# Performance work log

Measured on AMD Instinct MI355X. Metric: run time of the kernel, lower is better.

## Reference

```python
import jax, jax.numpy as jnp
import numpy as np

NP_CONST = 48.0  # Np in the original code


def dft_matrices(freq=48, time=512):
    # A[t, f] = exp(-2j*pi*t*f/time)/sqrt(time), split into re/im, shape [time, freq]
    t = np.arange(time)[:, None]
    f = np.arange(freq)[None, :]
    ang = -2.0 * np.pi * t * f / time
    scale = 1.0 / np.sqrt(time)
    return (np.cos(ang) * scale).astype(np.float32), (np.sin(ang) * scale).astype(np.float32)


def _mm(xr, xi, wr, wi):
    # complex matmul: (xr + i xi) @ (wr + i wi)
    return xr @ wr - xi @ wi, xr @ wi + xi @ wr


def _act(R, sigma, theta):
    # scaled soft-threshold (standard LAMP shrinkage); returns f and df/dR
    lam = theta[0] * sigma
    mag = jnp.abs(R)
    shr = jnp.maximum(mag - lam, 0.0)
    f = theta[1] * jnp.sign(R) * shr
    df = theta[1] * (mag > lam).astype(R.dtype)
    return f, df


def setup_inputs() -> dict:
    key = jax.random.key(0)
    L, B = 8, 8192
    dre, dim = dft_matrices(48, 512)
    u = jax.random.normal(key, (B, 48, 2), dtype=jnp.float32)
    # per-layer params initialized to the DFT matrices (as in LAMP_layer.__init__)
    A_re = jnp.broadcast_to(jnp.asarray(dre), (L, 512, 48)).copy()
    A_im = jnp.broadcast_to(jnp.asarray(dim), (L, 512, 48)).copy()
    theta = jnp.broadcast_to(jnp.array([1.0, 1.0, -1.0], dtype=jnp.float32), (L, 3)).copy()
    return {"u": u, "A_re": A_re, "A_im": A_im, "theta": theta,
            "DFT_re": jnp.asarray(dre), "DFT_im": jnp.asarray(dim)}


def _lamp_forward(u, A_re, A_im, theta, DFT_re, DFT_im):
    u_re, u_im = u[:, :, 0], u[:, :, 1]          # [B, 48]
    B = u_re.shape[0]
    z_re, z_im = u_re, u_im
    H_re = jnp.zeros((B, 512), dtype=u.dtype)
    H_im = jnp.zeros((B, 512), dtype=u.dtype)

    def layer(carry, params):
        z_re, z_im, H_re, H_im = carry
        Are, Aim, th = params                      # [512,48], [512,48], [3]
        # Z = z @ A.T : [B,48] x [48,512]
        Z_re, Z_im = _mm(z_re, z_im, Are.T, Aim.T)
        R_re = H_re + Z_re
        R_im = H_im + Z_im
        sigma = jnp.sqrt(jnp.sum(z_re * z_re) + jnp.sum(z_im * z_im)) / jnp.sqrt(NP_CONST)
        Hn_re, d_re = _act(R_re, sigma, th)
        Hn_im, d_im = _act(R_im, sigma, th)
        b_re = d_re.sum() / NP_CONST
        b_im = d_im.sum() / NP_CONST
        # h_hat = H_hat @ A : [B,512] x [512,48]
        h_re, h_im = _mm(Hn_re, Hn_im, Are, Aim)
        zn_re = u_re - h_re + b_re * z_re
        zn_im = u_im - h_im + b_im * z_im
        return (zn_re, zn_im, Hn_re, Hn_im), None

    (z_re, z_im, H_re, H_im), _ = jax.lax.scan(layer, (z_re, z_im, H_re, H_im),
                                               (A_re, A_im, theta))
    h_re, h_im = _mm(H_re, H_im, DFT_re, DFT_im)   # [B, 48]
    return jnp.stack((h_re, h_im), axis=2)          # [B, 48, 2]


def reference(u, A_re, A_im, theta, DFT_re, DFT_im):
    return _lamp_forward(u, A_re, A_im, theta, DFT_re, DFT_im)
```

## Files before the change

kernel.cpp:

```cpp
#include <hip/hip_runtime.h>
#include <hip/hip_bf16.h>
#include <math.h>

#define B_   8192
#define F_   48
#define T_   512
#define L_   8
#define NBLK 512
#define THR  256
#define NW   4
#define RPB  16
#define HST  520
#define ZS   52

typedef unsigned short ushort_t;
typedef unsigned int   uint_t;
typedef __attribute__((ext_vector_type(8))) short short8;
typedef __attribute__((ext_vector_type(4))) float f32x4;

#define MFMA(a,b,c) __builtin_amdgcn_mfma_f32_16x16x32_bf16(a,b,c,0,0,0)

__device__ inline ushort_t f2bf(float x) {
    __hip_bfloat16 h = __float2bfloat16(x);
    return *reinterpret_cast<ushort_t*>(&h);
}
__device__ inline float bf2f(ushort_t x) {
    __hip_bfloat16 h;
    *reinterpret_cast<ushort_t*>(&h) = x;
    return __bfloat162float(h);
}
__device__ inline short8 negbf(short8 v) {
    short8 r;
    #pragma unroll
    for (int i = 0; i < 8; ++i) r[i] = v[i] ^ (short)0x8000;
    return r;
}
__device__ inline short8 pack8(float4 a, float4 b) {
    short8 r;
    r[0]=(short)f2bf(a.x); r[1]=(short)f2bf(a.y); r[2]=(short)f2bf(a.z); r[3]=(short)f2bf(a.w);
    r[4]=(short)f2bf(b.x); r[5]=(short)f2bf(b.y); r[6]=(short)f2bf(b.z); r[7]=(short)f2bf(b.w);
    return r;
}

template<int NQ>
__device__ inline void reduce_vals(float* v, float* redL, int wave, int lane) {
    #pragma unroll
    for (int s = 32; s > 0; s >>= 1)
        #pragma unroll
        for (int q = 0; q < NQ; ++q) v[q] += __shfl_xor(v[q], s, 64);
    __syncthreads();
    if (lane == 0)
        #pragma unroll
        for (int q = 0; q < NQ; ++q) redL[q * NW + wave] = v[q];
    __syncthreads();
}

__device__ inline void bar_add(uint_t* cnt, int blk) {
    __hip_atomic_fetch_add(&cnt[(blk & 15) * 32], 1u, __ATOMIC_RELEASE, __HIP_MEMORY_SCOPE_AGENT);
}
__device__ inline void bar_wait(uint_t* cnt, uint_t tgt) {
    if (threadIdx.x == 0) {
        for (;;) {
            uint_t s = 0;
            #pragma unroll
            for (int i = 0; i < 16; ++i)
                s += __hip_atomic_load(&cnt[i * 32], __ATOMIC_RELAXED, __HIP_MEMORY_SCOPE_AGENT);
            if (s >= tgt) break;
            __builtin_amdgcn_s_sleep(2);
        }
        (void)__hip_atomic_load(&cnt[0], __ATOMIC_ACQUIRE, __HIP_MEMORY_SCOPE_AGENT);
    }
    __syncthreads();
}
__device__ inline float aload(const float* p) {
    return __hip_atomic_load(p, __ATOMIC_RELAXED, __HIP_MEMORY_SCOPE_AGENT);
}
__device__ inline void astore(float* p, float v) {
    __hip_atomic_store(p, v, __ATOMIC_RELAXED, __HIP_MEMORY_SCOPE_AGENT);
}

__device__ inline uint_t act2(uint_t v, float lam, float th1, float& cnt_) {
    float lo = __uint_as_float(v << 16);
    float hi = __uint_as_float(v & 0xffff0000u);
    float ml = fabsf(lo), mh = fabsf(hi);
    float fl = th1 * copysignf(fmaxf(ml - lam, 0.f), lo);
    float fh = th1 * copysignf(fmaxf(mh - lam, 0.f), hi);
    cnt_ += ((ml > lam) ? 1.f : 0.f) + ((mh > lam) ? 1.f : 0.f);
    return ((uint_t)f2bf(fl)) | (((uint_t)f2bf(fh)) << 16);
}

__global__ __launch_bounds__(256) void k_pre(
    const float* __restrict__ Ar, const float* __restrict__ Ai,
    const float* __restrict__ Dr, const float* __restrict__ Di,
    ushort_t* __restrict__ Afr, ushort_t* __restrict__ Afi,
    ushort_t* __restrict__ Atr, ushort_t* __restrict__ Ati,
    ushort_t* __restrict__ Dfr, ushort_t* __restrict__ Dfi,
    uint_t* __restrict__ cnt)
{
    const int gt = blockIdx.x * 256 + threadIdx.x;
    const int gs = gridDim.x * 256;
    if (gt < 512) cnt[gt] = 0u;
    for (int idx = gt; idx < L_ * 32768; idx += gs) {
        int j = idx & 7, rest = idx >> 3;
        int mm = rest & 15; rest >>= 4;
        int qq = rest & 3;  rest >>= 2;
        int k2 = rest & 1;  rest >>= 1;
        int tile = rest & 31;
        int l = rest >> 5;
        int t = tile * 16 + mm, k = k2 * 32 + qq * 8 + j;
        float vr = 0.f, vi = 0.f;
        if (k < 48) { int g = l * 24576 + t * 48 + k; vr = Ar[g]; vi = Ai[g]; }
        Afr[idx] = f2bf(vr); Afi[idx] = f2bf(vi);
    }
    for (int idx = gt; idx < L_ * 24576; idx += gs) {
        int j = idx & 7, rest = idx >> 3;
        int mm = rest & 15; rest >>= 4;
        int qq = rest & 3;  rest >>= 2;
        int ks = rest & 15; rest >>= 4;
        int ft = rest % 3;
        int l = rest / 3;
        int f = ft * 16 + mm, k = ks * 32 + qq * 8 + j;
        int g = l * 24576 + k * 48 + f;
        Atr[idx] = f2bf(Ar[g]); Ati[idx] = f2bf(Ai[g]);
    }
    for (int idx = gt; idx < 24576; idx += gs) {
        int j = idx & 7, rest = idx >> 3;
        int mm = rest & 15; rest >>= 4;
        int qq = rest & 3;  rest >>= 2;
        int ks = rest & 15;
        int ft = rest >> 4;
        int f = ft * 16 + mm, k = ks * 32 + qq * 8 + j;
        Dfr[idx] = f2bf(Dr[k * 48 + f]); Dfi[idx] = f2bf(Di[k * 48 + f]);
    }
}

__device__ inline void fwd_gemm(const ushort_t* Aflr, const ushort_t* Afli,
    const float* zreL, const float* zimL, ushort_t* HreL, ushort_t* HimL,
    int wave, int lane, int quad, int m, bool addH)
{
    const float* zpr = zreL + m * ZS;
    const float* zpi = zimL + m * ZS;
    short8 zr0 = pack8(*(const float4*)(zpr + quad * 8), *(const float4*)(zpr + quad * 8 + 4));
    short8 zi0 = pack8(*(const float4*)(zpi + quad * 8), *(const float4*)(zpi + quad * 8 + 4));
    short8 zr1 = {0,0,0,0,0,0,0,0}, zi1 = {0,0,0,0,0,0,0,0};
    if (quad < 2) {
        zr1 = pack8(*(const float4*)(zpr + 32 + quad * 8), *(const float4*)(zpr + 36 + quad * 8));
        zi1 = pack8(*(const float4*)(zpi + 32 + quad * 8), *(const float4*)(zpi + 36 + quad * 8));
    }
    short8 zin0 = negbf(zi0), zin1 = negbf(zi1);
    #pragma unroll
    for (int ct = 0; ct < 8; ++ct) {
        const int tile = wave * 8 + ct;
        const ushort_t* rp = Aflr + (size_t)(tile * 2) * 512 + lane * 8;
        const ushort_t* ip = Afli + (size_t)(tile * 2) * 512 + lane * 8;
        short8 ar0 = *(const short8*)rp;
        short8 ar1 = *(const short8*)(rp + 512);
        short8 ai0 = *(const short8*)ip;
        short8 ai1 = *(const short8*)(ip + 512);
        f32x4 accR = {0.f,0.f,0.f,0.f}, accI = {0.f,0.f,0.f,0.f};
        accR = MFMA(zr0, ar0, accR);
        accR = MFMA(zr1, ar1, accR);
        accR = MFMA(zin0, ai0, accR);
        accR = MFMA(zin1, ai1, accR);
        accI = MFMA(zr0, ai0, accI);
        accI = MFMA(zr1, ai1, accI);
        accI = MFMA(zi0, ar0, accI);
        accI = MFMA(zi1, ar1, accI);
        const int t = tile * 16 + m;
        #pragma unroll
        for (int reg = 0; reg < 4; ++reg) {
            const int lr = quad * 4 + reg;
            float Rr = accR[reg], Ri = accI[reg];
            if (addH) { Rr += bf2f(HreL[lr * HST + t]); Ri += bf2f(HimL[lr * HST + t]); }
            HreL[lr * HST + t] = f2bf(Rr);
            HimL[lr * HST + t] = f2bf(Ri);
        }
    }
    __syncthreads();
}

__global__ __launch_bounds__(THR, 2) void k_lamp(
    const float* __restrict__ u,
    const ushort_t* __restrict__ Afr, const ushort_t* __restrict__ Afi,
    const ushort_t* __restrict__ Atr, const ushort_t* __restrict__ Ati,
    const ushort_t* __restrict__ Dfr, const ushort_t* __restrict__ Dfi,
    const float* __restrict__ th,
    float* part, uint_t* cnt,
    float* __restrict__ out)
{
    extern __shared__ char dyn[];
    float*    pR   = (float*)dyn;
    float*    pI   = pR + 2 * 3 * 16 * 17;
    float*    zreL = pI + 2 * 3 * 16 * 17;
    float*    zimL = zreL + RPB * ZS;
    float*    redL = zimL + RPB * ZS;
    ushort_t* HreL = (ushort_t*)(redL + 32);
    ushort_t* HimL = HreL + RPB * HST;

    const int tid = threadIdx.x, blk = blockIdx.x;
    const int row0 = blk * RPB;
    const int wave = tid >> 6, lane = tid & 63;
    const int quad = lane >> 4, m = lane & 15;
    const int kq = wave;
    const float2* u2 = (const float2*)u;
    uint_t tgt = NBLK;

    {
        float acc = 0.f;
        #pragma unroll
        for (int k3 = 0; k3 < 3; ++k3) {
            int j = tid + k3 * THR;
            int r = j / 48, c = j - r * 48;
            float2 v = u2[(row0 + r) * 48 + c];
            zreL[r * ZS + c] = v.x; zimL[r * ZS + c] = v.y;
            acc += v.x * v.x + v.y * v.y;
        }
        float v[1] = {acc};
        reduce_vals<1>(v, redL, wave, lane);
        if (tid == 0) {
            float t0 = redL[0] + redL[1] + redL[2] + redL[3];
            astore(&part[blk * 8], t0);
        }
        __syncthreads();
        if (tid == 0) bar_add(cnt, blk);
    }

    fwd_gemm(Afr, Afi, zreL, zimL, HreL, HimL, wave, lane, quad, m, false);

    bar_wait(cnt, tgt);
    float lam, th1;
    {
        float v[1];
        v[0] = aload(&part[tid * 8]) + aload(&part[(tid + 256) * 8]);
        reduce_vals<1>(v, redL, wave, lane);
        float sig2 = redL[0] + redL[1] + redL[2] + redL[3];
        lam = th[0] * sqrtf(sig2 * (1.0f / 48.0f));
        th1 = th[1];
    }

    float dR[3], dI[3];
    for (int l = 0; l < L_; ++l) {
        float cr = 0.f, ci = 0.f;
        {
            uint4* Hr4 = (uint4*)HreL;
            uint4* Hi4 = (uint4*)HimL;
            #pragma unroll
            for (int k4 = 0; k4 < 4; ++k4) {
                int j = tid + k4 * THR;
                int r = j >> 6, c4 = j & 63;
                uint4* pr = Hr4 + r * 65 + c4;
                uint4* pi = Hi4 + r * 65 + c4;
                uint4 xr = *pr, xi = *pi;
                xr.x = act2(xr.x, lam, th1, cr); xr.y = act2(xr.y, lam, th1, cr);
                xr.z = act2(xr.z, lam, th1, cr); xr.w = act2(xr.w, lam, th1, cr);
                xi.x = act2(xi.x, lam, th1, ci); xi.y = act2(xi.y, lam, th1, ci);
                xi.z = act2(xi.z, lam, th1, ci); xi.w = act2(xi.w, lam, th1, ci);
                *pr = xr; *pi = xi;
            }
        }
        __syncthreads();
        if (l == L_ - 1) break;

        {
            const ushort_t* Atlr = Atr + (size_t)l * 24576;
            const ushort_t* Atli = Ati + (size_t)l * 24576;
            f32x4 aR[3], aI[3];
            #pragma unroll
            for (int q = 0; q < 3; ++q) { aR[q] = (f32x4){0,0,0,0}; aI[q] = (f32x4){0,0,0,0}; }
            #pragma unroll
            for (int ks = 0; ks < 4; ++ks) {
                const int ksa = kq * 4 + ks;
                const int k0 = ksa * 32 + quad * 8;
                short8 hr = *(const short8*)&HreL[m * HST + k0];
                short8 hi = *(const short8*)&HimL[m * HST + k0];
                short8 hin = negbf(hi);
                #pragma unroll
                for (int ft = 0; ft < 3; ++ft) {
                    short8 br = *(const short8*)(Atlr + (size_t)((ft * 16 + ksa) * 64 + lane) * 8);
                    short8 bi = *(const short8*)(Atli + (size_t)((ft * 16 + ksa) * 64 + lane) * 8);
                    aR[ft] = MFMA(hr, br, aR[ft]);
                    aR[ft] = MFMA(hin, bi, aR[ft]);
                    aI[ft] = MFMA(hr, bi, aI[ft]);
                    aI[ft] = MFMA(hi, br, aI[ft]);
                }
            }
            const int s = kq & 1;
            if (kq < 2) {
                #pragma unroll
                for (int ft = 0; ft < 3; ++ft)
                    #pragma unroll
                    for (int reg = 0; reg < 4; ++reg) {
                        pR[((s * 3 + ft) * 16 + quad * 4 + reg) * 17 + m] = aR[ft][reg];
                        pI[((s * 3 + ft) * 16 + quad * 4 + reg) * 17 + m] = aI[ft][reg];
                    }
            }
            __syncthreads();
            if (kq >= 2) {
                #pragma unroll
                for (int ft = 0; ft < 3; ++ft)
                    #pragma unroll
                    for (int reg = 0; reg < 4; ++reg) {
                        pR[((s * 3 + ft) * 16 + quad * 4 + reg) * 17 + m] += aR[ft][reg];
                        pI[((s * 3 + ft) * 16 + quad * 4 + reg) * 17 + m] += aI[ft][reg];
                    }
            }
            __syncthreads();
        }

        float S1 = 0.f, S2r = 0.f, S2i = 0.f, S3r = 0.f, S3i = 0.f;
        #pragma unroll
        for (int k3 = 0; k3 < 3; ++k3) {
            int j = tid + k3 * THR;
            int r = j / 48, f = j - r * 48;
            int ft = f >> 4, c = f & 15;
            float hR = pR[(ft * 16 + r) * 17 + c] + pR[((3 + ft) * 16 + r) * 17 + c];
            float hI = pI[(ft * 16 + r) * 17 + c] + pI[((3 + ft) * 16 + r) * 17 + c];
            float2 uv = u2[(row0 + r) * 48 + f];
            float zr = zreL[r * ZS + f], zi = zimL[r * ZS + f];
            float dr = uv.x - hR, di = uv.y - hI;
            dR[k3] = dr; dI[k3] = di;
            S1  += dr * dr + di * di;
            S2r += dr * zr; S2i += di * zi;
            S3r += zr * zr; S3i += zi * zi;
        }
        {
            float v[7] = {cr, ci, S1, S2r, S2i, S3r, S3i};
            reduce_vals<7>(v, redL, wave, lane);
            if (tid < 7) {
                float t0 = redL[tid * NW] + redL[tid * NW + 1] + redL[tid * NW + 2] + redL[tid * NW + 3];
                astore(&part[blk * 8 + tid], t0);
            }
            __syncthreads();
            if (tid == 0) bar_add(cnt, blk);
            tgt += NBLK;
        }
        bar_wait(cnt, tgt);
        float bre, bim;
        {
            float v[7];
            #pragma unroll
            for (int q = 0; q < 7; ++q)
                v[q] = aload(&part[tid * 8 + q]) + aload(&part[(tid + 256) * 8 + q]);
            reduce_vals<7>(v, redL, wave, lane);
            float tot[7];
            #pragma unroll
            for (int q = 0; q < 7; ++q)
                tot[q] = redL[q * NW] + redL[q * NW + 1] + redL[q * NW + 2] + redL[q * NW + 3];
            bre = th1 * tot[0] * (1.0f / 48.0f);
            bim = th1 * tot[1] * (1.0f / 48.0f);
            float sig2 = tot[2] + 2.f * bre * tot[3] + 2.f * bim * tot[4]
                       + bre * bre * tot[5] + bim * bim * tot[6];
            lam = th[(l + 1) * 3] * sqrtf(sig2 * (1.0f / 48.0f));
            th1 = th[(l + 1) * 3 + 1];
        }
        #pragma unroll
        for (int k3 = 0; k3 < 3; ++k3) {
            int j = tid + k3 * THR;
            int r = j / 48, f = j - r * 48;
            float zr = zreL[r * ZS + f], zi = zimL[r * ZS + f];
            zreL[r * ZS + f] = dR[k3] + bre * zr;
            zimL[r * ZS + f] = dI[k3] + bim * zi;
        }
        __syncthreads();
        fwd_gemm(Afr + (size_t)(l + 1) * 32768, Afi + (size_t)(l + 1) * 32768,
                 zreL, zimL, HreL, HimL, wave, lane, quad, m, true);
    }

    {
        f32x4 fR[3], fI[3];
        #pragma unroll
        for (int q = 0; q < 3; ++q) { fR[q] = (f32x4){0,0,0,0}; fI[q] = (f32x4){0,0,0,0}; }
        #pragma unroll
        for (int ks = 0; ks < 4; ++ks) {
            const int ksa = kq * 4 + ks;
            const int k0 = ksa * 32 + quad * 8;
            short8 hr = *(const short8*)&HreL[m * HST + k0];
            short8 hi = *(const short8*)&HimL[m * HST + k0];
            short8 hin = negbf(hi);
            #pragma unroll
            for (int ft = 0; ft < 3; ++ft) {
                short8 br = *(const short8*)(Dfr + (size_t)((ft * 16 + ksa) * 64 + lane) * 8);
                short8 bi = *(const short8*)(Dfi + (size_t)((ft * 16 + ksa) * 64 + lane) * 8);
                fR[ft] = MFMA(hr, br, fR[ft]);
                fR[ft] = MFMA(hin, bi, fR[ft]);
                fI[ft] = MFMA(hr, bi, fI[ft]);
                fI[ft] = MFMA(hi, br, fI[ft]);
            }
        }
        const int s = kq & 1;
        if (kq < 2) {
            #pragma unroll
            for (int ft = 0; ft < 3; ++ft)
                #pragma unroll
                for (int reg = 0; reg < 4; ++reg) {
                    pR[((s * 3 + ft) * 16 + quad * 4 + reg) * 17 + m] = fR[ft][reg];
                    pI[((s * 3 + ft) * 16 + quad * 4 + reg) * 17 + m] = fI[ft][reg];
                }
        }
        __syncthreads();
        if (kq >= 2) {
            #pragma unroll
            for (int ft = 0; ft < 3; ++ft)
                #pragma unroll
                for (int reg = 0; reg < 4; ++reg) {
                    pR[((s * 3 + ft) * 16 + quad * 4 + reg) * 17 + m] += fR[ft][reg];
                    pI[((s * 3 + ft) * 16 + quad * 4 + reg) * 17 + m] += fI[ft][reg];
                }
        }
        __syncthreads();
        float2* out2 = (float2*)out;
        #pragma unroll
        for (int k3 = 0; k3 < 3; ++k3) {
            int j = tid + k3 * THR;
            int r = j / 48, f = j - r * 48;
            int ft = f >> 4, c = f & 15;
            float hR = pR[(ft * 16 + r) * 17 + c] + pR[((3 + ft) * 16 + r) * 17 + c];
            float hI = pI[(ft * 16 + r) * 17 + c] + pI[((3 + ft) * 16 + r) * 17 + c];
            out2[(row0 + r) * 48 + f] = make_float2(hR, hI);
        }
    }
}

extern "C" void kernel_launch(void* const* d_in, const int* in_sizes, int n_in,
                              void* d_out, int out_size, void* d_ws, size_t ws_size,
                              hipStream_t stream) {
    (void)in_sizes; (void)n_in; (void)out_size; (void)ws_size;
    const float* u  = (const float*)d_in[0];
    const float* Ar = (const float*)d_in[1];
    const float* Ai = (const float*)d_in[2];
    const float* th = (const float*)d_in[3];
    const float* Dr = (const float*)d_in[4];
    const float* Di = (const float*)d_in[5];
    float* out = (float*)d_out;

    char* p = (char*)d_ws;
    auto alloc = [&](size_t bytes) -> char* {
        char* r = p;
        p += (bytes + 255) & ~(size_t)255;
        return r;
    };
    float*    part = (float*)alloc((size_t)NBLK * 8 * 4);
    uint_t*   cnt  = (uint_t*)alloc(512 * 4);
    ushort_t* Afr = (ushort_t*)alloc((size_t)L_ * 32768 * 2);
    ushort_t* Afi = (ushort_t*)alloc((size_t)L_ * 32768 * 2);
    ushort_t* Atr = (ushort_t*)alloc((size_t)L_ * 24576 * 2);
    ushort_t* Ati = (ushort_t*)alloc((size_t)L_ * 24576 * 2);
    ushort_t* Dfr = (ushort_t*)alloc((size_t)24576 * 2);
    ushort_t* Dfi = (ushort_t*)alloc((size_t)24576 * 2);

    k_pre<<<256, 256, 0, stream>>>(Ar, Ai, Dr, Di, Afr, Afi, Atr, Ati, Dfr, Dfi, cnt);

    const uint_t lds_bytes = 53120;
    hipFuncSetAttribute((const void*)k_lamp,
                        hipFuncAttributeMaxDynamicSharedMemorySize, (int)lds_bytes);
    void* args[] = { (void*)&u, (void*)&Afr, (void*)&Afi, (void*)&Atr, (void*)&Ati,
                     (void*)&Dfr, (void*)&Dfi, (void*)&th,
                     (void*)&part, (void*)&cnt, (void*)&out };
    hipLaunchCooperativeKernel((void*)k_lamp, dim3(NBLK), dim3(THR), args,
                               lds_bytes, stream);
}
```

Before: 292.1 us.

## Split forward GEMM by linearity to overlap with grid barrier wait

The new z is d + b·z, so the forward product is split into a d·A part computed before the grid-wide barrier wait and a (b·z)·A part computed after the scalars b are known. This hides barrier latency behind MFMA work. The soft-threshold activation is also fused into the epilogue of the second GEMM, which removes a separate pass over H in LDS. In exchange the forward GEMM runs twice per layer, there are extra bf16 roundings of H and of the partial operands, and LDS use grows, which could affect occupancy at two blocks per CU.

```diff
diff --git a/kernel.cpp b/kernel.cpp
--- a/kernel.cpp
+++ b/kernel.cpp
@@ -134,9 +134,9 @@
     }
 }
 
-__device__ inline void fwd_gemm(const ushort_t* Aflr, const ushort_t* Afli,
+__device__ inline void fwd_gemm0(const ushort_t* Aflr, const ushort_t* Afli,
     const float* zreL, const float* zimL, ushort_t* HreL, ushort_t* HimL,
-    int wave, int lane, int quad, int m, bool addH)
+    int wave, int lane, int quad, int m)
 {
     const float* zpr = zreL + m * ZS;
     const float* zpi = zimL + m * ZS;
@@ -170,10 +170,8 @@
         #pragma unroll
         for (int reg = 0; reg < 4; ++reg) {
             const int lr = quad * 4 + reg;
-            float Rr = accR[reg], Ri = accI[reg];
-            if (addH) { Rr += bf2f(HreL[lr * HST + t]); Ri += bf2f(HimL[lr * HST + t]); }
-            HreL[lr * HST + t] = f2bf(Rr);
-            HimL[lr * HST + t] = f2bf(Ri);
+            HreL[lr * HST + t] = f2bf(accR[reg]);
+            HimL[lr * HST + t] = f2bf(accI[reg]);
         }
     }
     __syncthreads();
@@ -194,7 +192,11 @@
     float*    zreL = pI + 2 * 3 * 16 * 17;
     float*    zimL = zreL + RPB * ZS;
     float*    redL = zimL + RPB * ZS;
-    ushort_t* HreL = (ushort_t*)(redL + 32);
+    ushort_t* dbr  = (ushort_t*)(redL + 32);
+    ushort_t* dbi  = dbr + 16 * 64;
+    ushort_t* zbr  = dbi + 16 * 64;
+    ushort_t* zbi  = zbr + 16 * 64;
+    ushort_t* HreL = zbi + 16 * 64;
     ushort_t* HimL = HreL + RPB * HST;
 
     const int tid = threadIdx.x, blk = blockIdx.x;
@@ -206,26 +208,28 @@
     uint_t tgt = NBLK;
 
     {
+        int r = tid >> 4, c = 48 + (tid & 15);
+        dbr[r * 64 + c] = 0; dbi[r * 64 + c] = 0;
+        zbr[r * 64 + c] = 0; zbi[r * 64 + c] = 0;
         float acc = 0.f;
         #pragma unroll
         for (int k3 = 0; k3 < 3; ++k3) {
             int j = tid + k3 * THR;
-            int r = j / 48, c = j - r * 48;
-            float2 v = u2[(row0 + r) * 48 + c];
-            zreL[r * ZS + c] = v.x; zimL[r * ZS + c] = v.y;
+            int rr = j / 48, cc = j - rr * 48;
+            float2 v = u2[(row0 + rr) * 48 + cc];
+            zreL[rr * ZS + cc] = v.x; zimL[rr * ZS + cc] = v.y;
             acc += v.x * v.x + v.y * v.y;
         }
         float v[1] = {acc};
         reduce_vals<1>(v, redL, wave, lane);
         if (tid == 0) {
-            float t0 = redL[0] + redL[1] + redL[2] + redL[3];
-            astore(&part[blk * 8], t0);
+            astore(&part[blk * 8], redL[0] + redL[1] + redL[2] + redL[3]);
         }
         __syncthreads();
         if (tid == 0) bar_add(cnt, blk);
     }
 
-    fwd_gemm(Afr, Afi, zreL, zimL, HreL, HimL, wave, lane, quad, m, false);
+    fwd_gemm0(Afr, Afi, zreL, zimL, HreL, HimL, wave, lane, quad, m);
 
     bar_wait(cnt, tgt);
     float lam, th1;
@@ -238,29 +242,28 @@
         th1 = th[1];
     }
 
+    float cr = 0.f, ci = 0.f;
+    {
+        uint4* Hr4 = (uint4*)HreL;
+        uint4* Hi4 = (uint4*)HimL;
+        #pragma unroll
+        for (int k4 = 0; k4 < 4; ++k4) {
+            int j = tid + k4 * THR;
+            int r = j >> 6, c4 = j & 63;
+            uint4* pr = Hr4 + r * 65 + c4;
+            uint4* pi = Hi4 + r * 65 + c4;
+            uint4 xr = *pr, xi = *pi;
+            xr.x = act2(xr.x, lam, th1, cr); xr.y = act2(xr.y, lam, th1, cr);
+            xr.z = act2(xr.z, lam, th1, cr); xr.w = act2(xr.w, lam, th1, cr);
+            xi.x = act2(xi.x, lam, th1, ci); xi.y = act2(xi.y, lam, th1, ci);
+            xi.z = act2(xi.z, lam, th1, ci); xi.w = act2(xi.w, lam, th1, ci);
+            *pr = xr; *pi = xi;
+        }
+        __syncthreads();
+    }
+
     float dR[3], dI[3];
-    for (int l = 0; l < L_; ++l) {
-        float cr = 0.f, ci = 0.f;
-        {
-            uint4* Hr4 = (uint4*)HreL;
-            uint4* Hi4 = (uint4*)HimL;
-            #pragma unroll
-            for (int k4 = 0; k4 < 4; ++k4) {
-                int j = tid + k4 * THR;
-                int r = j >> 6, c4 = j & 63;
-                uint4* pr = Hr4 + r * 65 + c4;
-                uint4* pi = Hi4 + r * 65 + c4;
-                uint4 xr = *pr, xi = *pi;
-                xr.x = act2(xr.x, lam, th1, cr); xr.y = act2(xr.y, lam, th1, cr);
-                xr.z = act2(xr.z, lam, th1, cr); xr.w = act2(xr.w, lam, th1, cr);
-                xi.x = act2(xi.x, lam, th1, ci); xi.y = act2(xi.y, lam, th1, ci);
-                xi.z = act2(xi.z, lam, th1, ci); xi.w = act2(xi.w, lam, th1, ci);
-                *pr = xr; *pi = xi;
-            }
-        }
-        __syncthreads();
-        if (l == L_ - 1) break;
-
+    for (int l = 0; l < L_ - 1; ++l) {
         {
             const ushort_t* Atlr = Atr + (size_t)l * 24576;
             const ushort_t* Atli = Ati + (size_t)l * 24576;
@@ -319,6 +322,8 @@
             float zr = zreL[r * ZS + f], zi = zimL[r * ZS + f];
             float dr = uv.x - hR, di = uv.y - hI;
             dR[k3] = dr; dI[k3] = di;
+            dbr[r * 64 + f] = f2bf(dr);
+            dbi[r * 64 + f] = f2bf(di);
             S1  += dr * dr + di * di;
             S2r += dr * zr; S2i += di * zi;
             S3r += zr * zr; S3i += zi * zi;
@@ -334,6 +339,43 @@
             if (tid == 0) bar_add(cnt, blk);
             tgt += NBLK;
         }
+
+        {
+            const ushort_t* Aflr = Afr + (size_t)(l + 1) * 32768;
+            const ushort_t* Afli = Afi + (size_t)(l + 1) * 32768;
+            short8 dr0 = *(const short8*)&dbr[m * 64 + quad * 8];
+            short8 dr1 = *(const short8*)&dbr[m * 64 + 32 + quad * 8];
+            short8 di0 = *(const short8*)&dbi[m * 64 + quad * 8];
+            short8 di1 = *(const short8*)&dbi[m * 64 + 32 + quad * 8];
+            short8 din0 = negbf(di0), din1 = negbf(di1);
+            #pragma unroll
+            for (int ct = 0; ct < 8; ++ct) {
+                const int tile = wave * 8 + ct;
+                const ushort_t* rp = Aflr + (size_t)(tile * 2) * 512 + lane * 8;
+                const ushort_t* ip = Afli + (size_t)(tile * 2) * 512 + lane * 8;
+                short8 ar0 = *(const short8*)rp;
+                short8 ar1 = *(const short8*)(rp + 512);
+                short8 ai0 = *(const short8*)ip;
+                short8 ai1 = *(const short8*)(ip + 512);
+                f32x4 accR = {0.f,0.f,0.f,0.f}, accI = {0.f,0.f,0.f,0.f};
+                accR = MFMA(dr0, ar0, accR);
+                accR = MFMA(dr1, ar1, accR);
+                accR = MFMA(din0, ai0, accR);
+                accR = MFMA(din1, ai1, accR);
+                accI = MFMA(dr0, ai0, accI);
+                accI = MFMA(dr1, ai1, accI);
+                accI = MFMA(di0, ar0, accI);
+                accI = MFMA(di1, ar1, accI);
+                const int t = tile * 16 + m;
+                #pragma unroll
+                for (int reg = 0; reg < 4; ++reg) {
+                    const int lr = quad * 4 + reg;
+                    HreL[lr * HST + t] = f2bf(bf2f(HreL[lr * HST + t]) + accR[reg]);
+                    HimL[lr * HST + t] = f2bf(bf2f(HimL[lr * HST + t]) + accI[reg]);
+                }
+            }
+        }
+
         bar_wait(cnt, tgt);
         float bre, bim;
         {
@@ -353,17 +395,64 @@
             lam = th[(l + 1) * 3] * sqrtf(sig2 * (1.0f / 48.0f));
             th1 = th[(l + 1) * 3 + 1];
         }
+
         #pragma unroll
         for (int k3 = 0; k3 < 3; ++k3) {
             int j = tid + k3 * THR;
             int r = j / 48, f = j - r * 48;
             float zr = zreL[r * ZS + f], zi = zimL[r * ZS + f];
-            zreL[r * ZS + f] = dR[k3] + bre * zr;
-            zimL[r * ZS + f] = dI[k3] + bim * zi;
+            float zhr = bre * zr, zhi = bim * zi;
+            zbr[r * 64 + f] = f2bf(zhr);
+            zbi[r * 64 + f] = f2bf(zhi);
+            zreL[r * ZS + f] = dR[k3] + zhr;
+            zimL[r * ZS + f] = dI[k3] + zhi;
         }
         __syncthreads();
-        fwd_gemm(Afr + (size_t)(l + 1) * 32768, Afi + (size_t)(l + 1) * 32768,
-                 zreL, zimL, HreL, HimL, wave, lane, quad, m, true);
+
+        cr = 0.f; ci = 0.f;
+        {
+            const ushort_t* Aflr = Afr + (size_t)(l + 1) * 32768;
+            const ushort_t* Afli = Afi + (size_t)(l + 1) * 32768;
+            short8 zr0 = *(const short8*)&zbr[m * 64 + quad * 8];
+            short8 zr1 = *(const short8*)&zbr[m * 64 + 32 + quad * 8];
+            short8 zi0 = *(const short8*)&zbi[m * 64 + quad * 8];
+            short8 zi1 = *(const short8*)&zbi[m * 64 + 32 + quad * 8];
+            short8 zin0 = negbf(zi0), zin1 = negbf(zi1);
+            #pragma unroll
+            for (int ct = 0; ct < 8; ++ct) {
+                const int tile = wave * 8 + ct;
+                const ushort_t* rp = Aflr + (size_t)(tile * 2) * 512 + lane * 8;
+                const ushort_t* ip = Afli + (size_t)(tile * 2) * 512 + lane * 8;
+                short8 ar0 = *(const short8*)rp;
+                short8 ar1 = *(const short8*)(rp + 512);
+                short8 ai0 = *(const short8*)ip;
+                short8 ai1 = *(const short8*)(ip + 512);
+                f32x4 accR = {0.f,0.f,0.f,0.f}, accI = {0.f,0.f,0.f,0.f};
+                accR = MFMA(zr0, ar0, accR);
+                accR = MFMA(zr1, ar1, accR);
+                accR = MFMA(zin0, ai0, accR);
+                accR = MFMA(zin1, ai1, accR);
+                accI = MFMA(zr0, ai0, accI);
+                accI = MFMA(zr1, ai1, accI);
+                accI = MFMA(zi0, ar0, accI);
+                accI = MFMA(zi1, ar1, accI);
+                const int t = tile * 16 + m;
+                #pragma unroll
+                for (int reg = 0; reg < 4; ++reg) {
+                    const int lr = quad * 4 + reg;
+                    float Rr = bf2f(HreL[lr * HST + t]) + accR[reg];
+                    float Ri = bf2f(HimL[lr * HST + t]) + accI[reg];
+                    float mr = fabsf(Rr), mi = fabsf(Ri);
+                    float fr = th1 * copysignf(fmaxf(mr - lam, 0.f), Rr);
+                    float fi = th1 * copysignf(fmaxf(mi - lam, 0.f), Ri);
+                    cr += (mr > lam) ? 1.f : 0.f;
+                    ci += (mi > lam) ? 1.f : 0.f;
+                    HreL[lr * HST + t] = f2bf(fr);
+                    HimL[lr * HST + t] = f2bf(fi);
+                }
+            }
+            __syncthreads();
+        }
     }
 
     {
@@ -450,7 +539,7 @@
 
     k_pre<<<256, 256, 0, stream>>>(Ar, Ai, Dr, Di, Afr, Afi, Atr, Ati, Dfr, Dfi, cnt);
 
-    const uint_t lds_bytes = 53120;
+    const uint_t lds_bytes = 61312;
     hipFuncSetAttribute((const void*)k_lamp,
                         hipFuncAttributeMaxDynamicSharedMemorySize, (int)lds_bytes);
     void* args[] = { (void*)&u, (void*)&Afr, (void*)&Afi, (void*)&Atr, (void*)&Ati,
```

Result: faster. 279.1 us (-4.5%).

## Overlap forward GEMM with grid barrier via linearity split, fuse activation, use smaller blocks

Applied to the files above, without the earlier changes.

Uses linearity to split the forward GEMM of the next layer's z into two parts. The residual part (u - h) goes through the A-GEMM before the grid barrier, and the b*z part is added after the barrier, together with a fused soft-threshold activation. The backward GEMM is reorganized so each of three waves owns one output tile, which removes the two-stage LDS reduction. When occupancy allows, the kernel is templated to run 8 rows per block across 1024 blocks, with a wider sharded barrier counter. This trades twice the forward MFMA work per layer and extra bf16 rounding (from summing separately rounded parts) for hiding the barrier latency and gaining more parallelism.

```diff
diff --git a/kernel.cpp b/kernel.cpp
--- a/kernel.cpp
+++ b/kernel.cpp
@@ -6,12 +6,10 @@
 #define F_   48
 #define T_   512
 #define L_   8
-#define NBLK 512
 #define THR  256
 #define NW   4
-#define RPB  16
 #define HST  520
-#define ZS   52
+#define DST  72
 
 typedef unsigned short ushort_t;
 typedef unsigned int   uint_t;
@@ -35,12 +33,6 @@
     for (int i = 0; i < 8; ++i) r[i] = v[i] ^ (short)0x8000;
     return r;
 }
-__device__ inline short8 pack8(float4 a, float4 b) {
-    short8 r;
-    r[0]=(short)f2bf(a.x); r[1]=(short)f2bf(a.y); r[2]=(short)f2bf(a.z); r[3]=(short)f2bf(a.w);
-    r[4]=(short)f2bf(b.x); r[5]=(short)f2bf(b.y); r[6]=(short)f2bf(b.z); r[7]=(short)f2bf(b.w);
-    return r;
-}
 
 template<int NQ>
 __device__ inline void reduce_vals(float* v, float* redL, int wave, int lane) {
@@ -55,15 +47,18 @@
     __syncthreads();
 }
 
+template<int SH>
 __device__ inline void bar_add(uint_t* cnt, int blk) {
-    __hip_atomic_fetch_add(&cnt[(blk & 15) * 32], 1u, __ATOMIC_RELEASE, __HIP_MEMORY_SCOPE_AGENT);
-}
+    __hip_atomic_fetch_add(&cnt[(blk & (SH - 1)) * 32], 1u, __ATOMIC_RELEASE,
+                           __HIP_MEMORY_SCOPE_AGENT);
+}
+template<int SH>
 __device__ inline void bar_wait(uint_t* cnt, uint_t tgt) {
     if (threadIdx.x == 0) {
         for (;;) {
             uint_t s = 0;
             #pragma unroll
-            for (int i = 0; i < 16; ++i)
+            for (int i = 0; i < SH; ++i)
                 s += __hip_atomic_load(&cnt[i * 32], __ATOMIC_RELAXED, __HIP_MEMORY_SCOPE_AGENT);
             if (s >= tgt) break;
             __builtin_amdgcn_s_sleep(2);
@@ -99,7 +94,7 @@
 {
     const int gt = blockIdx.x * 256 + threadIdx.x;
     const int gs = gridDim.x * 256;
-    if (gt < 512) cnt[gt] = 0u;
+    if (gt < 1024) cnt[gt] = 0u;
     for (int idx = gt; idx < L_ * 32768; idx += gs) {
         int j = idx & 7, rest = idx >> 3;
         int mm = rest & 15; rest >>= 4;
@@ -134,19 +129,58 @@
     }
 }
 
-__device__ inline void fwd_gemm(const ushort_t* Aflr, const ushort_t* Afli,
-    const float* zreL, const float* zimL, ushort_t* HreL, ushort_t* HimL,
-    int wave, int lane, int quad, int m, bool addH)
+template<int RPB, bool ADDH>
+__device__ inline void gemmA(const ushort_t* Aflr, const ushort_t* Afli,
+    const ushort_t* dbr, const ushort_t* dbi, ushort_t* HreL, ushort_t* HimL,
+    int wave, int lane, int quad, int m)
 {
-    const float* zpr = zreL + m * ZS;
-    const float* zpi = zimL + m * ZS;
-    short8 zr0 = pack8(*(const float4*)(zpr + quad * 8), *(const float4*)(zpr + quad * 8 + 4));
-    short8 zi0 = pack8(*(const float4*)(zpi + quad * 8), *(const float4*)(zpi + quad * 8 + 4));
-    short8 zr1 = {0,0,0,0,0,0,0,0}, zi1 = {0,0,0,0,0,0,0,0};
-    if (quad < 2) {
-        zr1 = pack8(*(const float4*)(zpr + 32 + quad * 8), *(const float4*)(zpr + 36 + quad * 8));
-        zi1 = pack8(*(const float4*)(zpi + 32 + quad * 8), *(const float4*)(zpi + 36 + quad * 8));
-    }
+    short8 dr0 = *(const short8*)&dbr[m * DST + quad * 8];
+    short8 dr1 = *(const short8*)&dbr[m * DST + 32 + quad * 8];
+    short8 di0 = *(const short8*)&dbi[m * DST + quad * 8];
+    short8 di1 = *(const short8*)&dbi[m * DST + 32 + quad * 8];
+    short8 din0 = negbf(di0), din1 = negbf(di1);
+    #pragma unroll
+    for (int ct = 0; ct < 8; ++ct) {
+        const int tile = wave * 8 + ct;
+        const ushort_t* rp = Aflr + (size_t)(tile * 2) * 512 + lane * 8;
+        const ushort_t* ip = Afli + (size_t)(tile * 2) * 512 + lane * 8;
+        short8 ar0 = *(const short8*)rp;
+        short8 ar1 = *(const short8*)(rp + 512);
+        short8 ai0 = *(const short8*)ip;
+        short8 ai1 = *(const short8*)(ip + 512);
+        f32x4 accR = {0.f,0.f,0.f,0.f}, accI = {0.f,0.f,0.f,0.f};
+        accR = MFMA(dr0, ar0, accR);
+        accR = MFMA(dr1, ar1, accR);
+        accR = MFMA(din0, ai0, accR);
+        accR = MFMA(din1, ai1, accR);
+        accI = MFMA(dr0, ai0, accI);
+        accI = MFMA(dr1, ai1, accI);
+        accI = MFMA(di0, ar0, accI);
+        accI = MFMA(di1, ar1, accI);
+        const int t = tile * 16 + m;
+        #pragma unroll
+        for (int reg = 0; reg < 4; ++reg) {
+            const int lr = quad * 4 + reg;
+            if (RPB == 16 || lr < RPB) {
+                float Rr = accR[reg], Ri = accI[reg];
+                if (ADDH) { Rr += bf2f(HreL[lr * HST + t]); Ri += bf2f(HimL[lr * HST + t]); }
+                HreL[lr * HST + t] = f2bf(Rr);
+                HimL[lr * HST + t] = f2bf(Ri);
+            }
+        }
+    }
+}
+
+template<int RPB>
+__device__ inline void gemmB(const ushort_t* Aflr, const ushort_t* Afli,
+    const ushort_t* dbr, const ushort_t* dbi, ushort_t* HreL, ushort_t* HimL,
+    float lam, float th1, float& cr, float& ci,
+    int wave, int lane, int quad, int m)
+{
+    short8 zr0 = *(const short8*)&dbr[m * DST + quad * 8];
+    short8 zr1 = *(const short8*)&dbr[m * DST + 32 + quad * 8];
+    short8 zi0 = *(const short8*)&dbi[m * DST + quad * 8];
+    short8 zi1 = *(const short8*)&dbi[m * DST + 32 + quad * 8];
     short8 zin0 = negbf(zi0), zin1 = negbf(zi1);
     #pragma unroll
     for (int ct = 0; ct < 8; ++ct) {
@@ -170,15 +204,54 @@
         #pragma unroll
         for (int reg = 0; reg < 4; ++reg) {
             const int lr = quad * 4 + reg;
-            float Rr = accR[reg], Ri = accI[reg];
-            if (addH) { Rr += bf2f(HreL[lr * HST + t]); Ri += bf2f(HimL[lr * HST + t]); }
-            HreL[lr * HST + t] = f2bf(Rr);
-            HimL[lr * HST + t] = f2bf(Ri);
-        }
-    }
-    __syncthreads();
-}
-
+            if (RPB == 16 || lr < RPB) {
+                float Rr = bf2f(HreL[lr * HST + t]) + accR[reg];
+                float Ri = bf2f(HimL[lr * HST + t]) + accI[reg];
+                float mr = fabsf(Rr), mi = fabsf(Ri);
+                float fr = th1 * copysignf(fmaxf(mr - lam, 0.f), Rr);
+                float fi = th1 * copysignf(fmaxf(mi - lam, 0.f), Ri);
+                cr += (mr > lam) ? 1.f : 0.f;
+                ci += (mi > lam) ? 1.f : 0.f;
+                HreL[lr * HST + t] = f2bf(fr);
+                HimL[lr * HST + t] = f2bf(fi);
+            }
+        }
+    }
+}
+
+template<int RPB>
+__device__ inline void bwd_gemm(const ushort_t* Br, const ushort_t* Bi,
+    const ushort_t* HreL, const ushort_t* HimL, float* pR, float* pI,
+    int wave, int lane, int quad, int m)
+{
+    if (wave < 3) {
+        const int ft = wave;
+        f32x4 aR = {0.f,0.f,0.f,0.f}, aI = {0.f,0.f,0.f,0.f};
+        #pragma unroll
+        for (int ks = 0; ks < 16; ++ks) {
+            const int k0 = ks * 32 + quad * 8;
+            short8 hr = {0,0,0,0,0,0,0,0}, hi = {0,0,0,0,0,0,0,0};
+            if (RPB == 16 || m < RPB) {
+                hr = *(const short8*)&HreL[m * HST + k0];
+                hi = *(const short8*)&HimL[m * HST + k0];
+            }
+            short8 hin = negbf(hi);
+            short8 br = *(const short8*)(Br + (size_t)((ft * 16 + ks) * 64 + lane) * 8);
+            short8 bi = *(const short8*)(Bi + (size_t)((ft * 16 + ks) * 64 + lane) * 8);
+            aR = MFMA(hr, br, aR);
+            aR = MFMA(hin, bi, aR);
+            aI = MFMA(hr, bi, aI);
+            aI = MFMA(hi, br, aI);
+        }
+        #pragma unroll
+        for (int reg = 0; reg < 4; ++reg) {
+            pR[(ft * 16 + quad * 4 + reg) * 17 + m] = aR[reg];
+            pI[(ft * 16 + quad * 4 + reg) * 17 + m] = aI[reg];
+        }
+    }
+}
+
+template<int RPB>
 __global__ __launch_bounds__(THR, 2) void k_lamp(
     const float* __restrict__ u,
     const ushort_t* __restrict__ Afr, const ushort_t* __restrict__ Afi,
@@ -188,159 +261,145 @@
     float* part, uint_t* cnt,
     float* __restrict__ out)
 {
+    constexpr int NBLK  = B_ / RPB;
+    constexpr int SH    = (NBLK > 512) ? 32 : 16;
+    constexpr int PLOAD = NBLK / THR;
+    constexpr int NELEM = RPB * F_;
+    constexpr int ZPT   = (NELEM + THR - 1) / THR;
+    constexpr bool EXACT = (NELEM % THR) == 0;
+
     extern __shared__ char dyn[];
     float*    pR   = (float*)dyn;
-    float*    pI   = pR + 2 * 3 * 16 * 17;
-    float*    zreL = pI + 2 * 3 * 16 * 17;
-    float*    zimL = zreL + RPB * ZS;
-    float*    redL = zimL + RPB * ZS;
-    ushort_t* HreL = (ushort_t*)(redL + 32);
+    float*    pI   = pR + 3 * 16 * 17;
+    float*    redL = pI + 3 * 16 * 17;
+    ushort_t* dbr  = (ushort_t*)(redL + 32);
+    ushort_t* dbi  = dbr + 16 * DST;
+    ushort_t* HreL = dbi + 16 * DST;
     ushort_t* HimL = HreL + RPB * HST;
 
     const int tid = threadIdx.x, blk = blockIdx.x;
     const int row0 = blk * RPB;
     const int wave = tid >> 6, lane = tid & 63;
     const int quad = lane >> 4, m = lane & 15;
-    const int kq = wave;
     const float2* u2 = (const float2*)u;
     uint_t tgt = NBLK;
 
     {
+        uint_t* z32 = (uint_t*)dbr;
+        for (int i = tid; i < 16 * DST; i += THR) z32[i] = 0u;
+    }
+    __syncthreads();
+
+    float zR[ZPT], zI[ZPT], dRr[ZPT], dIr[ZPT];
+    {
         float acc = 0.f;
         #pragma unroll
-        for (int k3 = 0; k3 < 3; ++k3) {
-            int j = tid + k3 * THR;
-            int r = j / 48, c = j - r * 48;
-            float2 v = u2[(row0 + r) * 48 + c];
-            zreL[r * ZS + c] = v.x; zimL[r * ZS + c] = v.y;
-            acc += v.x * v.x + v.y * v.y;
+        for (int k = 0; k < ZPT; ++k) {
+            int j = tid + k * THR;
+            zR[k] = 0.f; zI[k] = 0.f;
+            if (EXACT || j < NELEM) {
+                int r = j / 48, f = j - r * 48;
+                float2 v = u2[(row0 + r) * 48 + f];
+                zR[k] = v.x; zI[k] = v.y;
+                dbr[r * DST + f] = f2bf(v.x);
+                dbi[r * DST + f] = f2bf(v.y);
+                acc += v.x * v.x + v.y * v.y;
+            }
         }
         float v[1] = {acc};
         reduce_vals<1>(v, redL, wave, lane);
-        if (tid == 0) {
-            float t0 = redL[0] + redL[1] + redL[2] + redL[3];
-            astore(&part[blk * 8], t0);
-        }
+        if (tid == 0) astore(&part[blk * 8], redL[0] + redL[1] + redL[2] + redL[3]);
         __syncthreads();
-        if (tid == 0) bar_add(cnt, blk);
-    }
-
-    fwd_gemm(Afr, Afi, zreL, zimL, HreL, HimL, wave, lane, quad, m, false);
-
-    bar_wait(cnt, tgt);
+        if (tid == 0) bar_add<SH>(cnt, blk);
+    }
+
+    gemmA<RPB, false>(Afr, Afi, dbr, dbi, HreL, HimL, wave, lane, quad, m);
+
+    bar_wait<SH>(cnt, tgt);
     float lam, th1;
     {
-        float v[1];
-        v[0] = aload(&part[tid * 8]) + aload(&part[(tid + 256) * 8]);
+        float v[1] = {0.f};
+        #pragma unroll
+        for (int i = 0; i < PLOAD; ++i) v[0] += aload(&part[(tid + i * THR) * 8]);
         reduce_vals<1>(v, redL, wave, lane);
         float sig2 = redL[0] + redL[1] + redL[2] + redL[3];
         lam = th[0] * sqrtf(sig2 * (1.0f / 48.0f));
         th1 = th[1];
     }
 
-    float dR[3], dI[3];
-    for (int l = 0; l < L_; ++l) {
-        float cr = 0.f, ci = 0.f;
-        {
-            uint4* Hr4 = (uint4*)HreL;
-            uint4* Hi4 = (uint4*)HimL;
-            #pragma unroll
-            for (int k4 = 0; k4 < 4; ++k4) {
-                int j = tid + k4 * THR;
-                int r = j >> 6, c4 = j & 63;
-                uint4* pr = Hr4 + r * 65 + c4;
-                uint4* pi = Hi4 + r * 65 + c4;
-                uint4 xr = *pr, xi = *pi;
-                xr.x = act2(xr.x, lam, th1, cr); xr.y = act2(xr.y, lam, th1, cr);
-                xr.z = act2(xr.z, lam, th1, cr); xr.w = act2(xr.w, lam, th1, cr);
-                xi.x = act2(xi.x, lam, th1, ci); xi.y = act2(xi.y, lam, th1, ci);
-                xi.z = act2(xi.z, lam, th1, ci); xi.w = act2(xi.w, lam, th1, ci);
-                *pr = xr; *pi = xi;
-            }
+    float cr = 0.f, ci = 0.f;
+    {
+        uint4* Hr4 = (uint4*)HreL;
+        uint4* Hi4 = (uint4*)HimL;
+        constexpr int IT0 = RPB * 64 / THR;
+        #pragma unroll
+        for (int k = 0; k < IT0; ++k) {
+            int j = tid + k * THR;
+            int r = j >> 6, c4 = j & 63;
+            uint4* pr = Hr4 + r * 65 + c4;
+            uint4* pi = Hi4 + r * 65 + c4;
+            uint4 xr = *pr, xi = *pi;
+            xr.x = act2(xr.x, lam, th1, cr); xr.y = act2(xr.y, lam, th1, cr);
+            xr.z = act2(xr.z, lam, th1, cr); xr.w = act2(xr.w, lam, th1, cr);
+            xi.x = act2(xi.x, lam, th1, ci); xi.y = act2(xi.y, lam, th1, ci);
+            xi.z = act2(xi.z, lam, th1, ci); xi.w = act2(xi.w, lam, th1, ci);
+            *pr = xr; *pi = xi;
         }
         __syncthreads();
-        if (l == L_ - 1) break;
-
-        {
-            const ushort_t* Atlr = Atr + (size_t)l * 24576;
-            const ushort_t* Atli = Ati + (size_t)l * 24576;
-            f32x4 aR[3], aI[3];
-            #pragma unroll
-            for (int q = 0; q < 3; ++q) { aR[q] = (f32x4){0,0,0,0}; aI[q] = (f32x4){0,0,0,0}; }
-            #pragma unroll
-            for (int ks = 0; ks < 4; ++ks) {
-                const int ksa = kq * 4 + ks;
-                const int k0 = ksa * 32 + quad * 8;
-                short8 hr = *(const short8*)&HreL[m * HST + k0];
-                short8 hi = *(const short8*)&HimL[m * HST + k0];
-                short8 hin = negbf(hi);
-                #pragma unroll
-                for (int ft = 0; ft < 3; ++ft) {
-                    short8 br = *(const short8*)(Atlr + (size_t)((ft * 16 + ksa) * 64 + lane) * 8);
-                    short8 bi = *(const short8*)(Atli + (size_t)((ft * 16 + ksa) * 64 + lane) * 8);
-                    aR[ft] = MFMA(hr, br, aR[ft]);
-                    aR[ft] = MFMA(hin, bi, aR[ft]);
-                    aI[ft] = MFMA(hr, bi, aI[ft]);
-                    aI[ft] = MFMA(hi, br, aI[ft]);
-                }
-            }
-            const int s = kq & 1;
-            if (kq < 2) {
-                #pragma unroll
-                for (int ft = 0; ft < 3; ++ft)
-                    #pragma unroll
-                    for (int reg = 0; reg < 4; ++reg) {
-                        pR[((s * 3 + ft) * 16 + quad * 4 + reg) * 17 + m] = aR[ft][reg];
-                        pI[((s * 3 + ft) * 16 + quad * 4 + reg) * 17 + m] = aI[ft][reg];
-                    }
-            }
-            __syncthreads();
-            if (kq >= 2) {
-                #pragma unroll
-                for (int ft = 0; ft < 3; ++ft)
-                    #pragma unroll
-                    for (int reg = 0; reg < 4; ++reg) {
-                        pR[((s * 3 + ft) * 16 + quad * 4 + reg) * 17 + m] += aR[ft][reg];
-                        pI[((s * 3 + ft) * 16 + quad * 4 + reg) * 17 + m] += aI[ft][reg];
-                    }
-            }
-            __syncthreads();
-        }
+    }
+
+    for (int l = 0; l < L_ - 1; ++l) {
+        bwd_gemm<RPB>(Atr + (size_t)l * 24576, Ati + (size_t)l * 24576,
+                      HreL, HimL, pR, pI, wave, lane, quad, m);
+        __syncthreads();
 
         float S1 = 0.f, S2r = 0.f, S2i = 0.f, S3r = 0.f, S3i = 0.f;
         #pragma unroll
-        for (int k3 = 0; k3 < 3; ++k3) {
-            int j = tid + k3 * THR;
-            int r = j / 48, f = j - r * 48;
-            int ft = f >> 4, c = f & 15;
-            float hR = pR[(ft * 16 + r) * 17 + c] + pR[((3 + ft) * 16 + r) * 17 + c];
-            float hI = pI[(ft * 16 + r) * 17 + c] + pI[((3 + ft) * 16 + r) * 17 + c];
-            float2 uv = u2[(row0 + r) * 48 + f];
-            float zr = zreL[r * ZS + f], zi = zimL[r * ZS + f];
-            float dr = uv.x - hR, di = uv.y - hI;
-            dR[k3] = dr; dI[k3] = di;
-            S1  += dr * dr + di * di;
-            S2r += dr * zr; S2i += di * zi;
-            S3r += zr * zr; S3i += zi * zi;
+        for (int k = 0; k < ZPT; ++k) {
+            int j = tid + k * THR;
+            dRr[k] = 0.f; dIr[k] = 0.f;
+            if (EXACT || j < NELEM) {
+                int r = j / 48, f = j - r * 48;
+                int ft = f >> 4, c = f & 15;
+                float hR = pR[(ft * 16 + r) * 17 + c];
+                float hI = pI[(ft * 16 + r) * 17 + c];
+                float2 uv = u2[(row0 + r) * 48 + f];
+                float dr = uv.x - hR, di = uv.y - hI;
+                dRr[k] = dr; dIr[k] = di;
+                dbr[r * DST + f] = f2bf(dr);
+                dbi[r * DST + f] = f2bf(di);
+                S1  += dr * dr + di * di;
+                S2r += dr * zR[k]; S2i += di * zI[k];
+                S3r += zR[k] * zR[k]; S3i += zI[k] * zI[k];
+            }
         }
         {
             float v[7] = {cr, ci, S1, S2r, S2i, S3r, S3i};
             reduce_vals<7>(v, redL, wave, lane);
             if (tid < 7) {
-                float t0 = redL[tid * NW] + redL[tid * NW + 1] + redL[tid * NW + 2] + redL[tid * NW + 3];
-                astore(&part[blk * 8 + tid], t0);
+                astore(&part[blk * 8 + tid],
+                       redL[tid * NW] + redL[tid * NW + 1] + redL[tid * NW + 2] + redL[tid * NW + 3]);
             }
             __syncthreads();
-            if (tid == 0) bar_add(cnt, blk);
+            if (tid == 0) bar_add<SH>(cnt, blk);
             tgt += NBLK;
         }
-        bar_wait(cnt, tgt);
+
+        gemmA<RPB, true>(Afr + (size_t)(l + 1) * 32768, Afi + (size_t)(l + 1) * 32768,
+                         dbr, dbi, HreL, HimL, wave, lane, quad, m);
+
+        bar_wait<SH>(cnt, tgt);
         float bre, bim;
         {
             float v[7];
             #pragma unroll
-            for (int q = 0; q < 7; ++q)
-                v[q] = aload(&part[tid * 8 + q]) + aload(&part[(tid + 256) * 8 + q]);
+            for (int q = 0; q < 7; ++q) v[q] = 0.f;
+            #pragma unroll
+            for (int i = 0; i < PLOAD; ++i) {
+                const float* pb = &part[(size_t)(tid + i * THR) * 8];
+                #pragma unroll
+                for (int q = 0; q < 7; ++q) v[q] += aload(pb + q);
+            }
             reduce_vals<7>(v, redL, wave, lane);
             float tot[7];
             #pragma unroll
@@ -353,70 +412,38 @@
             lam = th[(l + 1) * 3] * sqrtf(sig2 * (1.0f / 48.0f));
             th1 = th[(l + 1) * 3 + 1];
         }
-        #pragma unroll
-        for (int k3 = 0; k3 < 3; ++k3) {
-            int j = tid + k3 * THR;
-            int r = j / 48, f = j - r * 48;
-            float zr = zreL[r * ZS + f], zi = zimL[r * ZS + f];
-            zreL[r * ZS + f] = dR[k3] + bre * zr;
-            zimL[r * ZS + f] = dI[k3] + bim * zi;
+
+        #pragma unroll
+        for (int k = 0; k < ZPT; ++k) {
+            int j = tid + k * THR;
+            if (EXACT || j < NELEM) {
+                int r = j / 48, f = j - r * 48;
+                float zhr = bre * zR[k], zhi = bim * zI[k];
+                dbr[r * DST + f] = f2bf(zhr);
+                dbi[r * DST + f] = f2bf(zhi);
+                zR[k] = dRr[k] + zhr;
+                zI[k] = dIr[k] + zhi;
+            }
         }
         __syncthreads();
-        fwd_gemm(Afr + (size_t)(l + 1) * 32768, Afi + (size_t)(l + 1) * 32768,
-                 zreL, zimL, HreL, HimL, wave, lane, quad, m, true);
-    }
-
-    {
-        f32x4 fR[3], fI[3];
-        #pragma unroll
-        for (int q = 0; q < 3; ++q) { fR[q] = (f32x4){0,0,0,0}; fI[q] = (f32x4){0,0,0,0}; }
-        #pragma unroll
-        for (int ks = 0; ks < 4; ++ks) {
-            const int ksa = kq * 4 + ks;
-            const int k0 = ksa * 32 + quad * 8;
-            short8 hr = *(const short8*)&HreL[m * HST + k0];
-            short8 hi = *(const short8*)&HimL[m * HST + k0];
-            short8 hin = negbf(hi);
-            #pragma unroll
-            for (int ft = 0; ft < 3; ++ft) {
-                short8 br = *(const short8*)(Dfr + (size_t)((ft * 16 + ksa) * 64 + lane) * 8);
-                short8 bi = *(const short8*)(Dfi + (size_t)((ft * 16 + ksa) * 64 + lane) * 8);
-                fR[ft] = MFMA(hr, br, fR[ft]);
-                fR[ft] = MFMA(hin, bi, fR[ft]);
-                fI[ft] = MFMA(hr, bi, fI[ft]);
-                fI[ft] = MFMA(hi, br, fI[ft]);
-            }
-        }
-        const int s = kq & 1;
-        if (kq < 2) {
-            #pragma unroll
-            for (int ft = 0; ft < 3; ++ft)
-                #pragma unroll
-                for (int reg = 0; reg < 4; ++reg) {
-                    pR[((s * 3 + ft) * 16 + quad * 4 + reg) * 17 + m] = fR[ft][reg];
-                    pI[((s * 3 + ft) * 16 + quad * 4 + reg) * 17 + m] = fI[ft][reg];
-                }
-        }
+
+        cr = 0.f; ci = 0.f;
+        gemmB<RPB>(Afr + (size_t)(l + 1) * 32768, Afi + (size_t)(l + 1) * 32768,
+                   dbr, dbi, HreL, HimL, lam, th1, cr, ci, wave, lane, quad, m);
         __syncthreads();
-        if (kq >= 2) {
-            #pragma unroll
-            for (int ft = 0; ft < 3; ++ft)
-                #pragma unroll
-                for (int reg = 0; reg < 4; ++reg) {
-                    pR[((s * 3 + ft) * 16 + quad * 4 + reg) * 17 + m] += fR[ft][reg];
-                    pI[((s * 3 + ft) * 16 + quad * 4 + reg) * 17 + m] += fI[ft][reg];
-                }
-        }
-        __syncthreads();
-        float2* out2 = (float2*)out;
-        #pragma unroll
-        for (int k3 = 0; k3 < 3; ++k3) {
-            int j = tid + k3 * THR;
+    }
+
+    bwd_gemm<RPB>(Dfr, Dfi, HreL, HimL, pR, pI, wave, lane, quad, m);
+    __syncthreads();
+    float2* out2 = (float2*)out;
+    #pragma unroll
+    for (int k = 0; k < ZPT; ++k) {
+        int j = tid + k * THR;
+        if (EXACT || j < NELEM) {
             int r = j / 48, f = j - r * 48;
             int ft = f >> 4, c = f & 15;
-            float hR = pR[(ft * 16 + r) * 17 + c] + pR[((3 + ft) * 16 + r) * 17 + c];
-            float hI = pI[(ft * 16 + r) * 17 + c] + pI[((3 + ft) * 16 + r) * 17 + c];
-            out2[(row0 + r) * 48 + f] = make_float2(hR, hI);
+            out2[(row0 + r) * 48 + f] =
+                make_float2(pR[(ft * 16 + r) * 17 + c], pI[(ft * 16 + r) * 17 + c]);
         }
     }
 }
@@ -439,8 +466,8 @@
         p += (bytes + 255) & ~(size_t)255;
         return r;
     };
-    float*    part = (float*)alloc((size_t)NBLK * 8 * 4);
-    uint_t*   cnt  = (uint_t*)alloc(512 * 4);
+    float*    part = (float*)alloc((size_t)1024 * 8 * 4);
+    uint_t*   cnt  = (uint_t*)alloc(1024 * 4);
     ushort_t* Afr = (ushort_t*)alloc((size_t)L_ * 32768 * 2);
     ushort_t* Afi = (ushort_t*)alloc((size_t)L_ * 32768 * 2);
     ushort_t* Atr = (ushort_t*)alloc((size_t)L_ * 24576 * 2);
@@ -450,12 +477,24 @@
 
     k_pre<<<256, 256, 0, stream>>>(Ar, Ai, Dr, Di, Afr, Afi, Atr, Ati, Dfr, Dfi, cnt);
 
-    const uint_t lds_bytes = 53120;
-    hipFuncSetAttribute((const void*)k_lamp,
-                        hipFuncAttributeMaxDynamicSharedMemorySize, (int)lds_bytes);
+    const int lds8  = 6528 + 128 + 4608 + 8 * 2080;
+    const int lds16 = 6528 + 128 + 4608 + 16 * 2080;
+    hipFuncSetAttribute((const void*)k_lamp<8>,
+                        hipFuncAttributeMaxDynamicSharedMemorySize, lds8);
+    hipFuncSetAttribute((const void*)k_lamp<16>,
+                        hipFuncAttributeMaxDynamicSharedMemorySize, lds16);
+
     void* args[] = { (void*)&u, (void*)&Afr, (void*)&Afi, (void*)&Atr, (void*)&Ati,
                      (void*)&Dfr, (void*)&Dfi, (void*)&th,
                      (void*)&part, (void*)&cnt, (void*)&out };
-    hipLaunchCooperativeKernel((void*)k_lamp, dim3(NBLK), dim3(THR), args,
-                               lds_bytes, stream);
-}
+
+    int nb = 0;
+    hipOccupancyMaxActiveBlocksPerMultiprocessor(&nb, (const void*)k_lamp<8>, THR, (size_t)lds8);
+    if (nb >= 4) {
+        hipLaunchCooperativeKernel((void*)k_lamp<8>, dim3(1024), dim3(THR), args,
+                                   lds8, stream);
+    } else {
+        hipLaunchCooperativeKernel((void*)k_lamp<16>, dim3(512), dim3(THR), args,
+                                   lds16, stream);
+    }
+}
```

After: 301.8 us. 3.3% more time.
